# Optimization experiments

Measured on AMD Instinct MI355X. Metric: run time of the kernel, lower is better.

## Reference

```python
import jax, jax.numpy as jnp
import numpy as np

D_MODEL, N_HEADS, D_C, D_COMP, D_ROPE = 2048, 16, 512, 768, 64
D_HEAD = D_MODEL // N_HEADS  # 128
B, S = 2, 2048
ROPE_THETA = 10000.0


def _rope_cos_sin(seq_len, dim):
    # frequencies for pairwise complex rotation, dim = per-head rope dim (even)
    inv_freq = 1.0 / (ROPE_THETA ** (jnp.arange(0, dim, 2, dtype=jnp.float32) / dim))
    t = jnp.arange(seq_len, dtype=jnp.float32)
    ang = t[:, None] * inv_freq[None, :]  # [S, dim/2]
    return jnp.cos(ang), jnp.sin(ang)


def _apply_rope(x, cos, sin):
    # x: [B, S, H, dr]; rotate consecutive pairs (view_as_complex semantics)
    x1, x2 = x[..., 0::2], x[..., 1::2]
    c = cos[None, :, None, :]
    s = sin[None, :, None, :]
    y1 = x1 * c - x2 * s
    y2 = x1 * s + x2 * c
    return jnp.stack([y1, y2], axis=-1).reshape(x.shape)


def setup_inputs() -> dict:
    key = jax.random.key(0)
    ks = jax.random.split(key, 9)
    sc = 0.02
    return {
        "x": jax.random.normal(ks[0], (B, S, D_MODEL), jnp.float32),
        "Wd": jax.random.normal(ks[1], (D_MODEL, D_C), jnp.float32) * sc,
        "bd": jnp.zeros((D_C,), jnp.float32),
        "Wu": jax.random.normal(ks[2], (D_C, N_HEADS * D_HEAD), jnp.float32) * sc,
        "bu": jnp.zeros((N_HEADS * D_HEAD,), jnp.float32),
        "Wqd": jax.random.normal(ks[3], (D_MODEL, D_COMP), jnp.float32) * sc,
        "bqd": jnp.zeros((D_COMP,), jnp.float32),
        "Wqu": jax.random.normal(ks[4], (D_COMP, N_HEADS * D_HEAD), jnp.float32) * sc,
        "bqu": jnp.zeros((N_HEADS * D_HEAD,), jnp.float32),
        "Wqr": jax.random.normal(ks[5], (D_COMP, N_HEADS * D_ROPE), jnp.float32) * sc,
        "bqr": jnp.zeros((N_HEADS * D_ROPE,), jnp.float32),
        "Wkr": jax.random.normal(ks[6], (D_MODEL, N_HEADS * D_ROPE), jnp.float32) * sc,
        "bkr": jnp.zeros((N_HEADS * D_ROPE,), jnp.float32),
        "Wo": jax.random.normal(ks[7], (N_HEADS * D_HEAD, D_MODEL), jnp.float32) * sc,
        "bo": jnp.zeros((D_MODEL,), jnp.float32),
    }


def reference(x, Wd, bd, Wu, bu, Wqd, bqd, Wqu, bqu, Wqr, bqr, Wkr, bkr, Wo, bo):
    b, s, _ = x.shape
    # low-rank KV compression
    kv_c = x @ Wd + bd                                   # [B,S,d_c]
    kv_up = (kv_c @ Wu + bu).reshape(b, s, N_HEADS, D_HEAD)  # shared K-content / V
    # low-rank Q compression
    q_cmp = x @ Wqd + bqd                                # [B,S,d_comp]
    q_c = (q_cmp @ Wqu + bqu).reshape(b, s, N_HEADS, D_HEAD)
    # decoupled RoPE branches
    cos, sin = _rope_cos_sin(s, D_ROPE)
    q_r = _apply_rope((q_cmp @ Wqr + bqr).reshape(b, s, N_HEADS, D_ROPE), cos, sin)
    k_r = _apply_rope((x @ Wkr + bkr).reshape(b, s, N_HEADS, D_ROPE), cos, sin)
    q = jnp.concatenate([q_c, q_r], axis=-1)             # [B,S,H,dh+dr]
    k = jnp.concatenate([kv_up, k_r], axis=-1)           # [B,S,H,dh+dr]
    scale = 1.0 / np.sqrt(D_HEAD).astype(np.float32)
    scores = jnp.einsum('bqhd,bkhd->bhqk', q, k) * scale  # [B,H,S,S]
    probs = jax.nn.softmax(scores, axis=-1)
    out = jnp.einsum('bhqk,bkhd->bqhd', probs, kv_up)    # v == kv_up (as in source)
    out = out.reshape(b, s, N_HEADS * D_HEAD)
    return out @ Wo + bo
```

## Files before the change

kernel.cpp:

```cpp
#include <hip/hip_runtime.h>
#include <cmath>

typedef __bf16 bf16;
typedef __bf16 bf16x8 __attribute__((ext_vector_type(8)));
typedef __bf16 bf16x4 __attribute__((ext_vector_type(4)));
typedef float f32x4 __attribute__((ext_vector_type(4)));
typedef int i32x4 __attribute__((ext_vector_type(4)));

#define S_LEN 2048
#define QK_LD 3072

__device__ __forceinline__ void async_copy16(const bf16* g, bf16* l) {
    __builtin_amdgcn_global_load_lds(
        (const __attribute__((address_space(1))) void*)g,
        (__attribute__((address_space(3))) void*)l, 16, 0, 0);
}

__global__ __launch_bounds__(256) void cast_f32_bf16(const float* __restrict__ in,
                                                     bf16* __restrict__ out) {
    size_t i = ((size_t)blockIdx.x * 256 + threadIdx.x) * 8;
    float4 a = *(const float4*)(in + i);
    float4 b = *(const float4*)(in + i + 4);
    bf16x8 v;
    v[0] = (bf16)a.x; v[1] = (bf16)a.y; v[2] = (bf16)a.z; v[3] = (bf16)a.w;
    v[4] = (bf16)b.x; v[5] = (bf16)b.y; v[6] = (bf16)b.z; v[7] = (bf16)b.w;
    *(bf16x8*)(out + i) = v;
}

__global__ __launch_bounds__(256) void transpose_cast(const float* __restrict__ W,
                                                      bf16* __restrict__ Wt,
                                                      int K, int N) {
    __shared__ float tile[64][68];
    int k0 = blockIdx.x * 64, n0 = blockIdx.y * 64;
    int t = threadIdx.x;
#pragma unroll
    for (int i = 0; i < 4; ++i) {
        int c = t + i * 256;
        int r = c >> 4, off = (c & 15) * 4;
        float4 v = *(const float4*)(W + (size_t)(k0 + r) * N + n0 + off);
        tile[r][off] = v.x; tile[r][off + 1] = v.y;
        tile[r][off + 2] = v.z; tile[r][off + 3] = v.w;
    }
    __syncthreads();
#pragma unroll
    for (int i = 0; i < 2; ++i) {
        int c = t + i * 256;
        int nr = c >> 3, koff = (c & 7) * 8;
        bf16x8 v;
#pragma unroll
        for (int j = 0; j < 8; ++j) v[j] = (bf16)tile[koff + j][nr];
        *(bf16x8*)(Wt + (size_t)(n0 + nr) * K + k0 + koff) = v;
    }
}

__global__ __launch_bounds__(256) void bias_cat(const float* __restrict__ bd,
                                                const float* __restrict__ bqd,
                                                const float* __restrict__ bkr,
                                                const float* __restrict__ bqu,
                                                const float* __restrict__ bqr,
                                                float* __restrict__ bcat) {
    int i = blockIdx.x * 256 + threadIdx.x;
    if (i < 512) bcat[i] = bd[i];
    else if (i < 1280) bcat[i] = bqd[i - 512];
    else if (i < 2304) bcat[i] = bkr[i - 1280];
    else if (i < 4352) bcat[i] = bqu[i - 2304];
    else if (i < 5376) bcat[i] = bqr[i - 4352];
}

__global__ __launch_bounds__(256) void rope_tab_k(float2* __restrict__ tab) {
    int id = blockIdx.x * 256 + threadIdx.x;
    int s = id >> 5, i = id & 31;
    float f = expf(-0.2878231366242557f * (float)i);
    float ang = (float)s * f;
    tab[id] = make_float2(cosf(ang), sinf(ang));
}

__global__ __launch_bounds__(256) void gemm_bt(const bf16* __restrict__ A, int lda,
                                               const bf16* __restrict__ Bt,
                                               const float* __restrict__ bias,
                                               void* __restrict__ out0,
                                               void* __restrict__ out1,
                                               int Ndim, int Kdim, int mode,
                                               const float2* __restrict__ tab) {
    __shared__ bf16 As[128 * 32];
    __shared__ bf16 Bs[128 * 32];
    int t = threadIdx.x;
    int bm = blockIdx.y, bn = blockIdx.x;
    int w = t >> 6, lane = t & 63;
    int wm = (w >> 1) * 64, wn = (w & 1) * 64;
    int l15 = lane & 15, q4 = lane >> 4;
    f32x4 acc[4][4] = {};

    int lrow = lane >> 2;
    int lcol = (lane & 3) * 8;
    int c0 = w * 2, c1 = w * 2 + 1;
    const bf16* aS0 = A  + (size_t)(bm * 128 + c0 * 16 + lrow) * lda + lcol;
    const bf16* aS1 = A  + (size_t)(bm * 128 + c1 * 16 + lrow) * lda + lcol;
    const bf16* bS0 = Bt + (size_t)(bn * 128 + c0 * 16 + lrow) * Kdim + lcol;
    const bf16* bS1 = Bt + (size_t)(bn * 128 + c1 * 16 + lrow) * Kdim + lcol;
    bf16* aD0 = &As[c0 * 512]; bf16* aD1 = &As[c1 * 512];
    bf16* bD0 = &Bs[c0 * 512]; bf16* bD1 = &Bs[c1 * 512];

    for (int kt = 0; kt < Kdim; kt += 32) {
        async_copy16(aS0 + kt, aD0);
        async_copy16(aS1 + kt, aD1);
        async_copy16(bS0 + kt, bD0);
        async_copy16(bS1 + kt, bD1);
        __syncthreads();
        bf16x8 af[4], bfr[4];
#pragma unroll
        for (int mb = 0; mb < 4; ++mb)
            af[mb] = *(const bf16x8*)&As[(wm + mb * 16 + l15) * 32 + q4 * 8];
#pragma unroll
        for (int nb = 0; nb < 4; ++nb)
            bfr[nb] = *(const bf16x8*)&Bs[(wn + nb * 16 + l15) * 32 + q4 * 8];
#pragma unroll
        for (int mb = 0; mb < 4; ++mb)
#pragma unroll
            for (int nb = 0; nb < 4; ++nb)
                acc[mb][nb] = __builtin_amdgcn_mfma_f32_16x16x32_bf16(
                    af[mb], bfr[nb], acc[mb][nb], 0, 0, 0);
        __syncthreads();
    }

#pragma unroll
    for (int mb = 0; mb < 4; ++mb) {
        int row = bm * 128 + wm + mb * 16 + q4 * 4;
#pragma unroll
        for (int nb = 0; nb < 4; ++nb) {
            int col = bn * 128 + wn + nb * 16 + l15;
            float bv = bias[col];
            if (mode == 1) {
#pragma unroll
                for (int r = 0; r < 4; ++r)
                    ((float*)out0)[(size_t)(row + r) * Ndim + col] = acc[mb][nb][r] + bv;
            } else if (mode == 4) {
                if (col < 1280) {
#pragma unroll
                    for (int r = 0; r < 4; ++r)
                        ((bf16*)out0)[(size_t)(row + r) * 2304 + col] =
                            (bf16)(acc[mb][nb][r] + bv);
                } else {
                    int rel = col - 1280;
                    int hh = rel >> 6, idx = rel & 63, ii = idx >> 1, odd = idx & 1;
#pragma unroll
                    for (int r = 0; r < 4; ++r) {
                        float vv = acc[mb][nb][r] + bv;
                        float pp = __shfl_xor(vv, 1, 64);
                        float2 cs = tab[((row + r) & 2047) * 32 + ii];
                        float o = vv * cs.x + (odd ? pp * cs.y : -pp * cs.y);
                        ((bf16*)out1)[(size_t)(row + r) * QK_LD + hh * 192 + 128 + idx] =
                            (bf16)o;
                    }
                }
            } else if (mode == 5) {
                if (col < 2048) {
                    int hh = col >> 7, dd = col & 127;
#pragma unroll
                    for (int r = 0; r < 4; ++r)
                        ((bf16*)out0)[(size_t)(row + r) * QK_LD + hh * 192 + dd] =
                            (bf16)(acc[mb][nb][r] + bv);
                } else {
                    int rel = col - 2048;
                    int hh = rel >> 6, idx = rel & 63, ii = idx >> 1, odd = idx & 1;
#pragma unroll
                    for (int r = 0; r < 4; ++r) {
                        float vv = acc[mb][nb][r] + bv;
                        float pp = __shfl_xor(vv, 1, 64);
                        float2 cs = tab[((row + r) & 2047) * 32 + ii];
                        float o = vv * cs.x + (odd ? pp * cs.y : -pp * cs.y);
                        ((bf16*)out0)[(size_t)(row + r) * QK_LD + hh * 192 + 128 + idx] =
                            (bf16)o;
                    }
                }
            } else {
                int hh = col >> 7, dd = col & 127;
                bf16x4 pack;
#pragma unroll
                for (int r = 0; r < 4; ++r) {
                    float vv = acc[mb][nb][r] + bv;
                    ((bf16*)out0)[(size_t)(row + r) * QK_LD + hh * 192 + dd] = (bf16)vv;
                    pack[r] = (bf16)vv;
                }
                int bidx = row >> 11, srow = row & 2047;
                *(bf16x4*)((bf16*)out1 +
                           ((size_t)(bidx * 16 + hh) * 128 + dd) * S_LEN + srow) = pack;
            }
        }
    }
}

__global__ __launch_bounds__(256, 2) void attn(const bf16* __restrict__ qbuf,
                                               const bf16* __restrict__ kbuf,
                                               const bf16* __restrict__ vt,
                                               bf16* __restrict__ attnout) {
    __shared__ bf16 Ks[64 * 200];
    __shared__ bf16 Vs[128 * 72];
    __shared__ bf16 Ps[128 * 72];
    int qt = blockIdx.x;
    int bh = blockIdx.y;
    int b = bh >> 4, h = bh & 15;
    int t = threadIdx.x, w = t >> 6, lane = t & 63;
    int l15 = lane & 15, q4 = lane >> 4;
    const float scale = 0.08838834764831845f;

    bf16x8 qf[2][6];
    {
        size_t base = (size_t)(b * S_LEN + qt * 128 + w * 32) * QK_LD + h * 192;
#pragma unroll
        for (int mb = 0; mb < 2; ++mb)
#pragma unroll
            for (int c = 0; c < 6; ++c)
                qf[mb][c] = *(const bf16x8*)(qbuf + base +
                            (size_t)(mb * 16 + l15) * QK_LD + c * 32 + q4 * 8);
    }

    f32x4 oacc[2][8] = {};
    float denom[2][4] = {};
    const bf16* kb_base = kbuf + (size_t)b * S_LEN * QK_LD + h * 192;
    const bf16* vt_base = vt + (size_t)bh * 128 * S_LEN;

    int kr_[6], ko_[6], vd_[4], vo_[4];
#pragma unroll
    for (int i = 0; i < 6; ++i) { int c = t + (i << 8); kr_[i] = c / 24; ko_[i] = (c % 24) * 8; }
#pragma unroll
    for (int i = 0; i < 4; ++i) { int c = t + (i << 8); vd_[i] = c >> 3; vo_[i] = (c & 7) * 8; }

    i32x4 kreg[6], vreg[4];
#pragma unroll
    for (int i = 0; i < 6; ++i)
        kreg[i] = *(const i32x4*)(kb_base + (size_t)kr_[i] * QK_LD + ko_[i]);
#pragma unroll
    for (int i = 0; i < 4; ++i)
        vreg[i] = *(const i32x4*)(vt_base + (size_t)vd_[i] * S_LEN + vo_[i]);

    for (int kt = 0; kt < 32; ++kt) {
        __syncthreads();
#pragma unroll
        for (int i = 0; i < 6; ++i) *(i32x4*)&Ks[kr_[i] * 200 + ko_[i]] = kreg[i];
#pragma unroll
        for (int i = 0; i < 4; ++i) *(i32x4*)&Vs[vd_[i] * 72 + vo_[i]] = vreg[i];
        __syncthreads();
        if (kt < 31) {
#pragma unroll
            for (int i = 0; i < 6; ++i)
                kreg[i] = *(const i32x4*)(kb_base +
                          (size_t)((kt + 1) * 64 + kr_[i]) * QK_LD + ko_[i]);
#pragma unroll
            for (int i = 0; i < 4; ++i)
                vreg[i] = *(const i32x4*)(vt_base +
                          (size_t)vd_[i] * S_LEN + (kt + 1) * 64 + vo_[i]);
        }

        f32x4 sacc[2][4] = {};
#pragma unroll
        for (int c = 0; c < 6; ++c) {
#pragma unroll
            for (int nk = 0; nk < 4; ++nk) {
                bf16x8 kb = *(const bf16x8*)&Ks[(nk * 16 + l15) * 200 + c * 32 + q4 * 8];
#pragma unroll
                for (int mb = 0; mb < 2; ++mb)
                    sacc[mb][nk] = __builtin_amdgcn_mfma_f32_16x16x32_bf16(
                        qf[mb][c], kb, sacc[mb][nk], 0, 0, 0);
            }
        }

#pragma unroll
        for (int mb = 0; mb < 2; ++mb)
#pragma unroll
            for (int nk = 0; nk < 4; ++nk)
#pragma unroll
                for (int r = 0; r < 4; ++r) {
                    float p = __expf(fminf(sacc[mb][nk][r] * scale, 50.0f));
                    denom[mb][r] += p;
                    Ps[(w * 32 + mb * 16 + q4 * 4 + r) * 72 + nk * 16 + l15] = (bf16)p;
                }

#pragma unroll
        for (int kc = 0; kc < 2; ++kc) {
            bf16x8 pa[2];
#pragma unroll
            for (int mb = 0; mb < 2; ++mb)
                pa[mb] = *(const bf16x8*)&Ps[(w * 32 + mb * 16 + l15) * 72 +
                                             kc * 32 + q4 * 8];
#pragma unroll
            for (int nb = 0; nb < 8; ++nb) {
                bf16x8 vb = *(const bf16x8*)&Vs[(nb * 16 + l15) * 72 + kc * 32 + q4 * 8];
#pragma unroll
                for (int mb = 0; mb < 2; ++mb)
                    oacc[mb][nb] = __builtin_amdgcn_mfma_f32_16x16x32_bf16(
                        pa[mb], vb, oacc[mb][nb], 0, 0, 0);
            }
        }
    }

#pragma unroll
    for (int off = 1; off < 16; off <<= 1)
#pragma unroll
        for (int mb = 0; mb < 2; ++mb)
#pragma unroll
            for (int r = 0; r < 4; ++r)
                denom[mb][r] += __shfl_xor(denom[mb][r], off, 64);

#pragma unroll
    for (int mb = 0; mb < 2; ++mb)
#pragma unroll
        for (int r = 0; r < 4; ++r) {
            float inv = 1.0f / denom[mb][r];
            int row = qt * 128 + w * 32 + mb * 16 + q4 * 4 + r;
#pragma unroll
            for (int nb = 0; nb < 8; ++nb) {
                int col = h * 128 + nb * 16 + l15;
                attnout[(size_t)(b * S_LEN + row) * 2048 + col] =
                    (bf16)(oacc[mb][nb][r] * inv);
            }
        }
}

extern "C" void kernel_launch(void* const* d_in, const int* in_sizes, int n_in,
                              void* d_out, int out_size, void* d_ws, size_t ws_size,
                              hipStream_t stream) {
    const float* x   = (const float*)d_in[0];
    const float* Wd  = (const float*)d_in[1];
    const float* bd  = (const float*)d_in[2];
    const float* Wu  = (const float*)d_in[3];
    const float* bu  = (const float*)d_in[4];
    const float* Wqd = (const float*)d_in[5];
    const float* bqd = (const float*)d_in[6];
    const float* Wqu = (const float*)d_in[7];
    const float* bqu = (const float*)d_in[8];
    const float* Wqr = (const float*)d_in[9];
    const float* bqr = (const float*)d_in[10];
    const float* Wkr = (const float*)d_in[11];
    const float* bkr = (const float*)d_in[12];
    const float* Wo  = (const float*)d_in[13];
    const float* bo  = (const float*)d_in[14];
    float* out = (float*)d_out;

    char* p = (char*)d_ws;
    auto alloc = [&](size_t n) { char* r = p; p += (n + 255) & ~(size_t)255; return r; };
    bf16* xb    = (bf16*)alloc((size_t)4096 * 2048 * 2);
    bf16* W1T   = (bf16*)alloc((size_t)2304 * 2048 * 2);
    bf16* W2T   = (bf16*)alloc((size_t)3072 * 768 * 2);
    bf16* WuT   = (bf16*)alloc((size_t)2048 * 512 * 2);
    bf16* WoT   = (bf16*)alloc((size_t)2048 * 2048 * 2);
    bf16* xproj = (bf16*)alloc((size_t)4096 * 2304 * 2);
    bf16* qbuf  = (bf16*)alloc((size_t)4096 * 3072 * 2);
    bf16* kbuf  = (bf16*)alloc((size_t)4096 * 3072 * 2);
    bf16* vt    = (bf16*)alloc((size_t)32 * 128 * 2048 * 2);
    bf16* aout  = (bf16*)alloc((size_t)4096 * 2048 * 2);
    float* bcat = (float*)alloc((size_t)5376 * 4);
    float2* tab = (float2*)alloc((size_t)65536 * 8);

    cast_f32_bf16<<<dim3(4096), dim3(256), 0, stream>>>(x, xb);
    transpose_cast<<<dim3(32, 8),  dim3(256), 0, stream>>>(Wd,  W1T,                        2048, 512);
    transpose_cast<<<dim3(32, 12), dim3(256), 0, stream>>>(Wqd, W1T + (size_t)512 * 2048,   2048, 768);
    transpose_cast<<<dim3(32, 16), dim3(256), 0, stream>>>(Wkr, W1T + (size_t)1280 * 2048,  2048, 1024);
    transpose_cast<<<dim3(12, 32), dim3(256), 0, stream>>>(Wqu, W2T,                        768,  2048);
    transpose_cast<<<dim3(12, 16), dim3(256), 0, stream>>>(Wqr, W2T + (size_t)2048 * 768,   768,  1024);
    transpose_cast<<<dim3(8, 32),  dim3(256), 0, stream>>>(Wu,  WuT,                        512,  2048);
    transpose_cast<<<dim3(32, 32), dim3(256), 0, stream>>>(Wo,  WoT,                        2048, 2048);
    bias_cat<<<dim3(21), dim3(256), 0, stream>>>(bd, bqd, bkr, bqu, bqr, bcat);
    rope_tab_k<<<dim3(256), dim3(256), 0, stream>>>(tab);

    gemm_bt<<<dim3(18, 32), dim3(256), 0, stream>>>(xb, 2048, W1T, bcat,
                                                    xproj, kbuf, 2304, 2048, 4, tab);
    gemm_bt<<<dim3(16, 32), dim3(256), 0, stream>>>(xproj, 2304, WuT, bu,
                                                    kbuf, vt, 2048, 512, 6, tab);
    gemm_bt<<<dim3(24, 32), dim3(256), 0, stream>>>(xproj + 512, 2304, W2T, bcat + 2304,
                                                    qbuf, nullptr, 3072, 768, 5, tab);

    attn<<<dim3(16, 32), dim3(256), 0, stream>>>(qbuf, kbuf, vt, aout);

    gemm_bt<<<dim3(16, 32), dim3(256), 0, stream>>>(aout, 2048, WoT, bo,
                                                    out, nullptr, 2048, 2048, 1, tab);
}
```

Baseline: 516.7 us.

## Merge setup launches, fuse up-projection GEMMs, and transpose attention score MFMA layout

Folds the seven weight transpose launches into one segmented kernel, and the bias-concat and rope-table kernels into one. The two up-projection GEMMs (Wu and Wq) run as a single launch that branches on block index. The attention kernel swaps its grid axes so blocks sharing a head run adjacently, and swaps the MFMA operands so each lane holds a transposed score tile. That layout lets probabilities be written to LDS as packed 4-wide stores and cuts the row-sum reduction to two shuffles plus a broadcast. These changes target launch overhead, low GPU occupancy from small grids, and scattered scalar LDS writes, at the cost of more index arithmetic and a risk of layout bugs in the transposed softmax path.

New measurement: 434.8 us. 15.9% less time.

```diff
diff --git a/kernel.cpp b/kernel.cpp
--- a/kernel.cpp
+++ b/kernel.cpp
@@ -27,17 +27,26 @@
     *(bf16x8*)(out + i) = v;
 }
 
-__global__ __launch_bounds__(256) void transpose_cast(const float* __restrict__ W,
-                                                      bf16* __restrict__ Wt,
-                                                      int K, int N) {
+struct TSeg { const float* src; bf16* dst; int K, N, blk0; };
+struct TArgs { TSeg s[7]; };
+
+__global__ __launch_bounds__(256) void transpose_all(TArgs a) {
     __shared__ float tile[64][68];
-    int k0 = blockIdx.x * 64, n0 = blockIdx.y * 64;
+    int b = blockIdx.x, si = 0;
+#pragma unroll
+    for (int i = 1; i < 7; ++i) if (b >= a.s[i].blk0) si = i;
+    TSeg sg = a.s[si];
+    int local = b - sg.blk0;
+    int kTiles = sg.K >> 6;
+    int kt = local % kTiles, nt = local / kTiles;
+    int k0 = kt * 64, n0 = nt * 64;
+    int K = sg.K, N = sg.N;
     int t = threadIdx.x;
 #pragma unroll
     for (int i = 0; i < 4; ++i) {
         int c = t + i * 256;
         int r = c >> 4, off = (c & 15) * 4;
-        float4 v = *(const float4*)(W + (size_t)(k0 + r) * N + n0 + off);
+        float4 v = *(const float4*)(sg.src + (size_t)(k0 + r) * N + n0 + off);
         tile[r][off] = v.x; tile[r][off + 1] = v.y;
         tile[r][off + 2] = v.z; tile[r][off + 3] = v.w;
     }
@@ -49,43 +58,42 @@
         bf16x8 v;
 #pragma unroll
         for (int j = 0; j < 8; ++j) v[j] = (bf16)tile[koff + j][nr];
-        *(bf16x8*)(Wt + (size_t)(n0 + nr) * K + k0 + koff) = v;
-    }
-}
-
-__global__ __launch_bounds__(256) void bias_cat(const float* __restrict__ bd,
-                                                const float* __restrict__ bqd,
-                                                const float* __restrict__ bkr,
-                                                const float* __restrict__ bqu,
-                                                const float* __restrict__ bqr,
-                                                float* __restrict__ bcat) {
-    int i = blockIdx.x * 256 + threadIdx.x;
-    if (i < 512) bcat[i] = bd[i];
-    else if (i < 1280) bcat[i] = bqd[i - 512];
-    else if (i < 2304) bcat[i] = bkr[i - 1280];
-    else if (i < 4352) bcat[i] = bqu[i - 2304];
-    else if (i < 5376) bcat[i] = bqr[i - 4352];
-}
-
-__global__ __launch_bounds__(256) void rope_tab_k(float2* __restrict__ tab) {
-    int id = blockIdx.x * 256 + threadIdx.x;
-    int s = id >> 5, i = id & 31;
-    float f = expf(-0.2878231366242557f * (float)i);
-    float ang = (float)s * f;
-    tab[id] = make_float2(cosf(ang), sinf(ang));
-}
-
-__global__ __launch_bounds__(256) void gemm_bt(const bf16* __restrict__ A, int lda,
-                                               const bf16* __restrict__ Bt,
-                                               const float* __restrict__ bias,
-                                               void* __restrict__ out0,
-                                               void* __restrict__ out1,
-                                               int Ndim, int Kdim, int mode,
-                                               const float2* __restrict__ tab) {
-    __shared__ bf16 As[128 * 32];
-    __shared__ bf16 Bs[128 * 32];
+        *(bf16x8*)(sg.dst + (size_t)(n0 + nr) * K + k0 + koff) = v;
+    }
+}
+
+__global__ __launch_bounds__(256) void setup_small(const float* __restrict__ bd,
+                                                   const float* __restrict__ bqd,
+                                                   const float* __restrict__ bkr,
+                                                   const float* __restrict__ bqu,
+                                                   const float* __restrict__ bqr,
+                                                   float* __restrict__ bcat,
+                                                   float2* __restrict__ tab) {
+    if (blockIdx.x < 21) {
+        int i = blockIdx.x * 256 + threadIdx.x;
+        if (i < 512) bcat[i] = bd[i];
+        else if (i < 1280) bcat[i] = bqd[i - 512];
+        else if (i < 2304) bcat[i] = bkr[i - 1280];
+        else if (i < 4352) bcat[i] = bqu[i - 2304];
+        else if (i < 5376) bcat[i] = bqr[i - 4352];
+    } else {
+        int id = (blockIdx.x - 21) * 256 + threadIdx.x;
+        int s = id >> 5, i = id & 31;
+        float f = expf(-0.2878231366242557f * (float)i);
+        float ang = (float)s * f;
+        tab[id] = make_float2(cosf(ang), sinf(ang));
+    }
+}
+
+__device__ __forceinline__ void gemm_core(const bf16* __restrict__ A, int lda,
+                                          const bf16* __restrict__ Bt,
+                                          const float* __restrict__ bias,
+                                          void* __restrict__ out0,
+                                          void* __restrict__ out1,
+                                          int Ndim, int Kdim, int mode,
+                                          const float2* __restrict__ tab,
+                                          int bn, int bm, bf16* As, bf16* Bs) {
     int t = threadIdx.x;
-    int bm = blockIdx.y, bn = blockIdx.x;
     int w = t >> 6, lane = t & 63;
     int wm = (w >> 1) * 64, wn = (w & 1) * 64;
     int l15 = lane & 15, q4 = lane >> 4;
@@ -190,6 +198,39 @@
     }
 }
 
+__global__ __launch_bounds__(256) void gemm_bt(const bf16* __restrict__ A, int lda,
+                                               const bf16* __restrict__ Bt,
+                                               const float* __restrict__ bias,
+                                               void* __restrict__ out0,
+                                               void* __restrict__ out1,
+                                               int Ndim, int Kdim, int mode,
+                                               const float2* __restrict__ tab) {
+    __shared__ bf16 As[128 * 32];
+    __shared__ bf16 Bs[128 * 32];
+    gemm_core(A, lda, Bt, bias, out0, out1, Ndim, Kdim, mode, tab,
+              blockIdx.x, blockIdx.y, As, Bs);
+}
+
+__global__ __launch_bounds__(256) void gemm_up(const bf16* __restrict__ xproj,
+                                               const bf16* __restrict__ WuT,
+                                               const float* __restrict__ bu,
+                                               void* __restrict__ kbuf,
+                                               void* __restrict__ vt,
+                                               const bf16* __restrict__ W2T,
+                                               const float* __restrict__ bq,
+                                               void* __restrict__ qbuf,
+                                               const float2* __restrict__ tab) {
+    __shared__ bf16 As[128 * 32];
+    __shared__ bf16 Bs[128 * 32];
+    int bn = blockIdx.x;
+    if (bn < 16)
+        gemm_core(xproj, 2304, WuT, bu, kbuf, vt, 2048, 512, 6, tab,
+                  bn, blockIdx.y, As, Bs);
+    else
+        gemm_core(xproj + 512, 2304, W2T, bq, qbuf, nullptr, 3072, 768, 5, tab,
+                  bn - 16, blockIdx.y, As, Bs);
+}
+
 __global__ __launch_bounds__(256, 2) void attn(const bf16* __restrict__ qbuf,
                                                const bf16* __restrict__ kbuf,
                                                const bf16* __restrict__ vt,
@@ -197,8 +238,8 @@
     __shared__ bf16 Ks[64 * 200];
     __shared__ bf16 Vs[128 * 72];
     __shared__ bf16 Ps[128 * 72];
-    int qt = blockIdx.x;
-    int bh = blockIdx.y;
+    int bh = blockIdx.x;
+    int qt = blockIdx.y;
     int b = bh >> 4, h = bh & 15;
     int t = threadIdx.x, w = t >> 6, lane = t & 63;
     int l15 = lane & 15, q4 = lane >> 4;
@@ -216,7 +257,7 @@
     }
 
     f32x4 oacc[2][8] = {};
-    float denom[2][4] = {};
+    float denom[2] = {0.f, 0.f};
     const bf16* kb_base = kbuf + (size_t)b * S_LEN * QK_LD + h * 192;
     const bf16* vt_base = vt + (size_t)bh * 128 * S_LEN;
 
@@ -261,20 +302,23 @@
 #pragma unroll
                 for (int mb = 0; mb < 2; ++mb)
                     sacc[mb][nk] = __builtin_amdgcn_mfma_f32_16x16x32_bf16(
-                        qf[mb][c], kb, sacc[mb][nk], 0, 0, 0);
+                        kb, qf[mb][c], sacc[mb][nk], 0, 0, 0);
             }
         }
 
 #pragma unroll
         for (int mb = 0; mb < 2; ++mb)
 #pragma unroll
-            for (int nk = 0; nk < 4; ++nk)
+            for (int nk = 0; nk < 4; ++nk) {
+                bf16x4 pk;
 #pragma unroll
                 for (int r = 0; r < 4; ++r) {
                     float p = __expf(fminf(sacc[mb][nk][r] * scale, 50.0f));
-                    denom[mb][r] += p;
-                    Ps[(w * 32 + mb * 16 + q4 * 4 + r) * 72 + nk * 16 + l15] = (bf16)p;
+                    denom[mb] += p;
+                    pk[r] = (bf16)p;
                 }
+                *(bf16x4*)&Ps[(w * 32 + mb * 16 + l15) * 72 + nk * 16 + q4 * 4] = pk;
+            }
 
 #pragma unroll
         for (int kc = 0; kc < 2; ++kc) {
@@ -295,18 +339,17 @@
     }
 
 #pragma unroll
-    for (int off = 1; off < 16; off <<= 1)
-#pragma unroll
-        for (int mb = 0; mb < 2; ++mb)
-#pragma unroll
-            for (int r = 0; r < 4; ++r)
-                denom[mb][r] += __shfl_xor(denom[mb][r], off, 64);
+    for (int mb = 0; mb < 2; ++mb) {
+        denom[mb] += __shfl_xor(denom[mb], 16, 64);
+        denom[mb] += __shfl_xor(denom[mb], 32, 64);
+    }
 
 #pragma unroll
     for (int mb = 0; mb < 2; ++mb)
 #pragma unroll
         for (int r = 0; r < 4; ++r) {
-            float inv = 1.0f / denom[mb][r];
+            float dv = __shfl(denom[mb], q4 * 4 + r, 64);
+            float inv = 1.0f / dv;
             int row = qt * 128 + w * 32 + mb * 16 + q4 * 4 + r;
 #pragma unroll
             for (int nb = 0; nb < 8; ++nb) {
@@ -353,24 +396,24 @@
     float2* tab = (float2*)alloc((size_t)65536 * 8);
 
     cast_f32_bf16<<<dim3(4096), dim3(256), 0, stream>>>(x, xb);
-    transpose_cast<<<dim3(32, 8),  dim3(256), 0, stream>>>(Wd,  W1T,                        2048, 512);
-    transpose_cast<<<dim3(32, 12), dim3(256), 0, stream>>>(Wqd, W1T + (size_t)512 * 2048,   2048, 768);
-    transpose_cast<<<dim3(32, 16), dim3(256), 0, stream>>>(Wkr, W1T + (size_t)1280 * 2048,  2048, 1024);
-    transpose_cast<<<dim3(12, 32), dim3(256), 0, stream>>>(Wqu, W2T,                        768,  2048);
-    transpose_cast<<<dim3(12, 16), dim3(256), 0, stream>>>(Wqr, W2T + (size_t)2048 * 768,   768,  1024);
-    transpose_cast<<<dim3(8, 32),  dim3(256), 0, stream>>>(Wu,  WuT,                        512,  2048);
-    transpose_cast<<<dim3(32, 32), dim3(256), 0, stream>>>(Wo,  WoT,                        2048, 2048);
-    bias_cat<<<dim3(21), dim3(256), 0, stream>>>(bd, bqd, bkr, bqu, bqr, bcat);
-    rope_tab_k<<<dim3(256), dim3(256), 0, stream>>>(tab);
+
+    TArgs ta;
+    ta.s[0] = {Wd,  W1T,                       2048, 512,  0};
+    ta.s[1] = {Wqd, W1T + (size_t)512 * 2048,  2048, 768,  256};
+    ta.s[2] = {Wkr, W1T + (size_t)1280 * 2048, 2048, 1024, 640};
+    ta.s[3] = {Wqu, W2T,                       768,  2048, 1152};
+    ta.s[4] = {Wqr, W2T + (size_t)2048 * 768,  768,  1024, 1536};
+    ta.s[5] = {Wu,  WuT,                       512,  2048, 1728};
+    ta.s[6] = {Wo,  WoT,                       2048, 2048, 1984};
+    transpose_all<<<dim3(3008), dim3(256), 0, stream>>>(ta);
+    setup_small<<<dim3(277), dim3(256), 0, stream>>>(bd, bqd, bkr, bqu, bqr, bcat, tab);
 
     gemm_bt<<<dim3(18, 32), dim3(256), 0, stream>>>(xb, 2048, W1T, bcat,
                                                     xproj, kbuf, 2304, 2048, 4, tab);
-    gemm_bt<<<dim3(16, 32), dim3(256), 0, stream>>>(xproj, 2304, WuT, bu,
-                                                    kbuf, vt, 2048, 512, 6, tab);
-    gemm_bt<<<dim3(24, 32), dim3(256), 0, stream>>>(xproj + 512, 2304, W2T, bcat + 2304,
-                                                    qbuf, nullptr, 3072, 768, 5, tab);
-
-    attn<<<dim3(16, 32), dim3(256), 0, stream>>>(qbuf, kbuf, vt, aout);
+    gemm_up<<<dim3(40, 32), dim3(256), 0, stream>>>(xproj, WuT, bu, kbuf, vt,
+                                                    W2T, bcat + 2304, qbuf, tab);
+
+    attn<<<dim3(32, 16), dim3(256), 0, stream>>>(qbuf, kbuf, vt, aout);
 
     gemm_bt<<<dim3(16, 32), dim3(256), 0, stream>>>(aout, 2048, WoT, bo,
                                                     out, nullptr, 2048, 2048, 1, tab);
```
